# Performance work log

Hardware: AMD Instinct MI355X
Metric: run time of the kernel (lower is better)

Reference implementation:

```python
import jax, jax.numpy as jnp
import numpy as np

T, B, IN, OUT = 32, 16, 64, 64
L, W, S = 4096, 64, 3          # mem_length, mem_width, shifting_size
READ_SIZE = W + 3 + S           # k, beta, g, gamma, s
WRITE_SIZE = W + 3 + S + 2 * W  # addressing params + erase + add


def setup_inputs() -> dict:
    key = jax.random.key(0)
    k1, k2 = jax.random.split(key)
    inputs = jax.random.normal(k1, (T, B, IN), dtype=jnp.float32)
    Wc = jax.random.normal(k2, (IN + OUT + W, OUT + READ_SIZE + WRITE_SIZE), dtype=jnp.float32) * 0.05
    bc = jnp.zeros((OUT + READ_SIZE + WRITE_SIZE,), dtype=jnp.float32)
    return {"inputs": inputs, "Wc": Wc, "bc": bc}


def _get_w(params, w_prev, memory):
    # params: [B, W+3+S]; w_prev: [B, L]; memory: [B, L, W]
    k = params[:, :W]
    beta = jax.nn.softplus(params[:, W])[:, None]
    g = jax.nn.sigmoid(params[:, W + 1])[:, None]
    gamma = jax.nn.softplus(params[:, W + 2])[:, None] + 1.0
    s = jax.nn.softmax(params[:, -S:], axis=-1)
    eps = 1e-14
    norm_k = jnp.sqrt(jnp.sum(k * k, axis=-1, keepdims=True) + eps)    # [B,1]
    norm_mem = jnp.sqrt(jnp.sum(memory * memory, axis=-1) + eps)       # [B,L]
    K = jnp.einsum('blw,bw->bl', memory, k) / (norm_mem * norm_k)      # cosine sim
    w_c = jax.nn.softmax(K * beta, axis=-1)
    w_g = w_c * g + (1.0 - g) * w_prev
    # circular shift: w_tilde[i] = sum_j s[j] * w_g[(i + j - left) mod L]
    left = S // 2
    shifted = jnp.stack([jnp.roll(w_g, left - j, axis=1) for j in range(S)], axis=-1)  # [B,L,S]
    w_tilde = jnp.einsum('bls,bs->bl', shifted, s)
    w = jnp.power(w_tilde, gamma)   # sharpen, gamma >= 1
    return w / jnp.sum(w, axis=1, keepdims=True)


def reference(inputs, Wc, bc):
    Bsz = inputs.shape[1]
    r0 = jnp.zeros((Bsz, W), jnp.float32)
    o0 = jnp.zeros((Bsz, OUT), jnp.float32)
    w0 = jnp.zeros((Bsz, L), jnp.float32).at[:, 0].set(1.0)  # one-hot init weights
    m0 = jnp.zeros((Bsz, L, W), jnp.float32)

    def step(carry, x_t):
        r, out, rw, ww, mem = carry
        co = jnp.concatenate([x_t, out, r], axis=1) @ Wc + bc  # linear controller
        out = co[:, :OUT]
        rp = co[:, OUT:OUT + READ_SIZE]
        wp = co[:, -WRITE_SIZE:]
        # read head (uses pre-write memory)
        rw = _get_w(rp, rw, mem)
        r = jnp.einsum('blw,bl->bw', mem, rw)
        # write head: address with same memory, then erase/add
        ww = _get_w(wp[:, :-2 * W], ww, mem)
        e = jax.nn.sigmoid(wp[:, -2 * W:-W])
        a = wp[:, -W:]
        mem = mem * (1.0 - ww[:, :, None] * e[:, None, :]) + ww[:, :, None] * a[:, None, :]
        return (r, out, rw, ww, mem), out

    _, outs = jax.lax.scan(step, (r0, o0, w0, w0, m0), inputs)
    return outs  # [T, B, OUT]
```

## Files before the change

kernel.cpp:

```cpp
#include <hip/hip_runtime.h>

#define T_STEPS 32
#define BATCH   16
#define NBPB    16
#define NBLK    (BATCH * NBPB)
#define NTHR    1024
#define LSL     256
#define MSTR    65
#define NIN     192
#define CO      332

#define OFF_CTR   0
#define OFF_SSUM  512
#define OFF_RSUM  (OFF_SSUM + BATCH * T_STEPS * 4)
#define OFF_HE    (OFF_RSUM + BATCH * T_STEPS * 64)
#define OFF_HP    (OFF_HE + BATCH * T_STEPS * NBPB * 4)
#define COMM_FLOATS (OFF_HP + BATCH * (T_STEPS + 1) * NBPB * 4)

__device__ __forceinline__ float waveSum(float v) {
#pragma unroll
  for (int off = 32; off > 0; off >>= 1) v += __shfl_xor(v, off, 64);
  return v;
}
__device__ __forceinline__ float sigmoidf(float x) { return 1.f / (1.f + __expf(-x)); }
__device__ __forceinline__ float softplusf(float x) { return x > 15.f ? x : log1pf(__expf(x)); }
__device__ __forceinline__ float aload(const float* p) {
  return __hip_atomic_load(p, __ATOMIC_RELAXED, __HIP_MEMORY_SCOPE_AGENT);
}
__device__ __forceinline__ void astore(float* p, float v) {
  __hip_atomic_store(p, v, __ATOMIC_RELAXED, __HIP_MEMORY_SCOPE_AGENT);
}

__device__ __forceinline__ void gbar(unsigned* c, unsigned expected) {
  __syncthreads();
  if (threadIdx.x == 0) {
    atomicAdd(c, 1u);
    while (__hip_atomic_load(c, __ATOMIC_RELAXED, __HIP_MEMORY_SCOPE_AGENT) < expected)
      __builtin_amdgcn_s_sleep(1);
  }
  __syncthreads();
}

__global__ void __launch_bounds__(NTHR, 1) ntm_kernel(
    const float* __restrict__ inp, const float* __restrict__ Wc,
    const float* __restrict__ bcv, float* __restrict__ dout,
    float* __restrict__ comm)
{
  const int b   = blockIdx.x & 15;
  const int g   = blockIdx.x >> 4;
  const int tid = threadIdx.x;
  const int wv  = tid >> 6;
  const int lane = tid & 63;

  __shared__ float mem[LSL * MSTR];
  __shared__ float wpR[LSL], wpW[LSL];
  __shared__ float wbR[LSL], wbW[LSL];
  __shared__ float erR[LSL], erW[LSL];
  __shared__ float xin[NIN], kr[64], kw[64], psc[12], elds[64], alds[64];
  __shared__ float outb[2][64], scrA[16], scrB[16], red[8], rpart[64];
  __shared__ float edge[8], coef[12];

  unsigned* ctr = (unsigned*)comm + b * 32;

  for (int i = tid; i < LSL * MSTR; i += NTHR) mem[i] = 0.f;
  if (tid < LSL) { wpR[tid] = 0.f; wpW[tid] = 0.f; }
  if (g == 0 && tid == 0) { wpR[0] = 1.f; wpW[0] = 1.f; }
  if (tid < 64) { outb[0][tid] = 0.f; outb[1][tid] = 0.f; }
  {
    float* hp0 = comm + OFF_HP + ((size_t)(b * (T_STEPS + 1) + 0) * NBPB + g) * 4;
    if (tid == 0)       { float v = (g == 0) ? 1.f : 0.f; astore(hp0 + 0, v); astore(hp0 + 2, v); }
    if (tid == LSL - 1) { astore(hp0 + 1, 0.f); astore(hp0 + 3, 0.f); }
  }
  unsigned expct = NBPB;
  gbar(ctr, expct);

  for (int t = 0; t < T_STEPS; ++t) {
    float* sS  = comm + OFF_SSUM + (size_t)(b * T_STEPS + t) * 4;
    float* rS  = comm + OFF_RSUM + (size_t)(b * T_STEPS + t) * 64;
    float* hE  = comm + OFF_HE + ((size_t)(b * T_STEPS + t) * NBPB + g) * 4;
    float* hPn = comm + OFF_HP + ((size_t)(b * (T_STEPS + 1) + t + 1) * NBPB + g) * 4;

    if (tid < 64)       xin[tid] = inp[((size_t)t * BATCH + b) * 64 + tid];
    else if (tid < 128) xin[tid] = outb[(t + 1) & 1][tid - 64];
    else if (tid < 192) {
      if (t == 0) xin[tid] = 0.f;
      else {
        const float* sP = comm + OFF_SSUM + (size_t)(b * T_STEPS + t - 1) * 4;
        const float* rP = comm + OFF_RSUM + (size_t)(b * T_STEPS + t - 1) * 64;
        xin[tid] = aload(rP + (tid - 128)) / aload(sP + 2);
      }
    }
    __syncthreads();

    if (tid < 2 * CO) {
      const int col = tid >> 1, h = tid & 1;
      float acc = h ? 0.f : bcv[col];
      const float* wcp = Wc + col + (size_t)(96 * h) * CO;
#pragma unroll 8
      for (int i = 0; i < 96; ++i) acc = fmaf(xin[96 * h + i], wcp[(size_t)i * CO], acc);
      acc += __shfl_xor(acc, 1, 64);
      if (h == 0) {
        if (col < 64) {
          outb[t & 1][col] = acc;
          if (g == 0) dout[((size_t)t * BATCH + b) * 64 + col] = acc;
        }
        else if (col < 128) kr[col - 64] = acc;
        else if (col < 134) psc[col - 128] = acc;
        else if (col < 198) kw[col - 134] = acc;
        else if (col < 204) psc[6 + (col - 198)] = acc;
        else if (col < 268) elds[col - 204] = sigmoidf(acc);
        else                alds[col - 268] = acc;
      }
    }
    __syncthreads();
    if (wv == 0)      { float v = kr[lane]; float s = waveSum(v * v); if (!lane) red[4] = 1.f / sqrtf(s + 1e-14f); }
    else if (wv == 1) { float v = kw[lane]; float s = waveSum(v * v); if (!lane) red[5] = 1.f / sqrtf(s + 1e-14f); }
    else if (wv == 2 && !lane) { red[6] = softplusf(psc[0]); red[7] = softplusf(psc[6]); }
    __syncthreads();

    {
      const float invnkR = red[4], invnkW = red[5];
      const float betaR = red[6], betaW = red[7];
      const int l = tid >> 2, h = tid & 3;
      const int base = l * MSTR + 16 * h;
      const float* krh = kr + 16 * h;
      const float* kwh = kw + 16 * h;
      float ss = 0.f, dr = 0.f, dw = 0.f;
#pragma unroll 8
      for (int i = 0; i < 16; ++i) {
        float v = mem[base + i];
        ss = fmaf(v, v, ss); dr = fmaf(v, krh[i], dr); dw = fmaf(v, kwh[i], dw);
      }
      ss += __shfl_xor(ss, 1, 64); ss += __shfl_xor(ss, 2, 64);
      dr += __shfl_xor(dr, 1, 64); dr += __shfl_xor(dr, 2, 64);
      dw += __shfl_xor(dw, 1, 64); dw += __shfl_xor(dw, 2, 64);
      float rinv = rsqrtf(ss + 1e-14f);
      float eRv = __expf(betaR * (dr * rinv * invnkR - 1.f));
      float eWv = __expf(betaW * (dw * rinv * invnkW - 1.f));
      if (h == 0) {
        erR[l] = eRv; erW[l] = eWv;
        if (l == 0)       { astore(hE + 0, eRv); astore(hE + 2, eWv); }
        if (l == LSL - 1) { astore(hE + 1, eRv); astore(hE + 3, eWv); }
      }
      float sRl = h ? 0.f : eRv, sWl = h ? 0.f : eWv;
      sRl = waveSum(sRl); sWl = waveSum(sWl);
      if (!lane) { scrA[wv] = sRl; scrB[wv] = sWl; }
      __syncthreads();
      if (tid == 0) {
        float a = 0.f, bb = 0.f;
        for (int j = 0; j < 16; ++j) { a += scrA[j]; bb += scrB[j]; }
        atomicAdd(sS + 0, a); atomicAdd(sS + 1, bb);
      }
    }
    expct += NBPB; gbar(ctr, expct);

    {
      const int gm = (g + NBPB - 1) & (NBPB - 1), gp = (g + 1) & (NBPB - 1);
      if (tid == 0) {
        float invSR = 1.f / aload(sS + 0), invSW = 1.f / aload(sS + 1);
        float gR = sigmoidf(psc[1]); coef[0] = gR * invSR; coef[1] = 1.f - gR;
        coef[2] = softplusf(psc[2]) + 1.f;
        float x0 = psc[3], x1 = psc[4], x2 = psc[5];
        float mx = fmaxf(x0, fmaxf(x1, x2));
        float e0 = __expf(x0 - mx), e1 = __expf(x1 - mx), e2 = __expf(x2 - mx);
        float es = 1.f / (e0 + e1 + e2);
        coef[3] = e0 * es; coef[4] = e1 * es; coef[5] = e2 * es;
        float gW = sigmoidf(psc[7]); coef[6] = gW * invSW; coef[7] = 1.f - gW;
        coef[8] = softplusf(psc[8]) + 1.f;
        float y0 = psc[9], y1 = psc[10], y2 = psc[11];
        float my = fmaxf(y0, fmaxf(y1, y2));
        float f0 = __expf(y0 - my), f1 = __expf(y1 - my), f2 = __expf(y2 - my);
        float fs = 1.f / (f0 + f1 + f2);
        coef[9] = f0 * fs; coef[10] = f1 * fs; coef[11] = f2 * fs;
      }
      if (tid == 1) {
        const float* hEm = comm + OFF_HE + ((size_t)(b * T_STEPS + t) * NBPB + gm) * 4;
        const float* hPm = comm + OFF_HP + ((size_t)(b * (T_STEPS + 1) + t) * NBPB + gm) * 4;
        edge[0] = aload(hEm + 1); edge[1] = aload(hEm + 3);
        edge[2] = aload(hPm + 1); edge[3] = aload(hPm + 3);
      }
      if (tid == 2) {
        const float* hEp = comm + OFF_HE + ((size_t)(b * T_STEPS + t) * NBPB + gp) * 4;
        const float* hPp = comm + OFF_HP + ((size_t)(b * (T_STEPS + 1) + t) * NBPB + gp) * 4;
        edge[4] = aload(hEp + 0); edge[5] = aload(hEp + 2);
        edge[6] = aload(hPp + 0); edge[7] = aload(hPp + 2);
      }
      __syncthreads();

      float pRl = 0.f, pWl = 0.f;
      if (tid < LSL) {
        const float aR = coef[0], bR = coef[1], gaR = coef[2];
        const float sr0 = coef[3], sr1 = coef[4], sr2 = coef[5];
        const float aW = coef[6], bW = coef[7], gaW = coef[8];
        const float sw0 = coef[9], sw1 = coef[10], sw2 = coef[11];

        float erm = tid ? erR[tid - 1] : edge[0];
        float ewm = tid ? erW[tid - 1] : edge[1];
        float prm = tid ? wpR[tid - 1] : edge[2];
        float pwm = tid ? wpW[tid - 1] : edge[3];
        float erp = (tid < LSL - 1) ? erR[tid + 1] : edge[4];
        float ewp = (tid < LSL - 1) ? erW[tid + 1] : edge[5];
        float prp = (tid < LSL - 1) ? wpR[tid + 1] : edge[6];
        float pwp = (tid < LSL - 1) ? wpW[tid + 1] : edge[7];

        float wgm = aR * erm + bR * prm;
        float wg0 = aR * erR[tid] + bR * wpR[tid];
        float wgp = aR * erp + bR * prp;
        float wR = __powf(sr0 * wgm + sr1 * wg0 + sr2 * wgp, gaR);
        float vgm = aW * ewm + bW * pwm;
        float vg0 = aW * erW[tid] + bW * wpW[tid];
        float vgp = aW * ewp + bW * pwp;
        float wW = __powf(sw0 * vgm + sw1 * vg0 + sw2 * vgp, gaW);
        wbR[tid] = wR; wbW[tid] = wW;
        pRl = wR; pWl = wW;
      }
      pRl = waveSum(pRl); pWl = waveSum(pWl);
      if (!lane && wv < 4) { scrA[wv] = pRl; scrB[wv] = pWl; }
      __syncthreads();
      if (tid == 0) {
        float a = 0.f, bb = 0.f;
        for (int j = 0; j < 4; ++j) { a += scrA[j]; bb += scrB[j]; }
        atomicAdd(sS + 2, a); atomicAdd(sS + 3, bb);
      }
      float wbv[4];
#pragma unroll
      for (int k = 0; k < 4; ++k) wbv[k] = wbR[lane + 64 * k];
#pragma unroll
      for (int r2 = 0; r2 < 4; ++r2) {
        const int w = wv * 4 + r2;
        float racc = 0.f;
#pragma unroll
        for (int k = 0; k < 4; ++k)
          racc = fmaf(mem[(lane + 64 * k) * MSTR + w], wbv[k], racc);
        racc = waveSum(racc);
        if (!lane) rpart[w] = racc;
      }
      __syncthreads();
      if (tid < 64) atomicAdd(rS + tid, rpart[tid]);
    }
    expct += NBPB; gbar(ctr, expct);

    {
      if (tid == 0) { red[2] = 1.f / aload(sS + 2); red[3] = 1.f / aload(sS + 3); }
      __syncthreads();
      if (tid < LSL) {
        float nR = wbR[tid] * red[2];
        float nW = wbW[tid] * red[3];
        wpR[tid] = nR; wpW[tid] = nW;
        if (tid == 0)       { astore(hPn + 0, nR); astore(hPn + 2, nW); }
        if (tid == LSL - 1) { astore(hPn + 1, nR); astore(hPn + 3, nW); }
      }
      __syncthreads();
      float wwv[4];
#pragma unroll
      for (int k = 0; k < 4; ++k) wwv[k] = wpW[lane + 64 * k];
#pragma unroll
      for (int r2 = 0; r2 < 4; ++r2) {
        const int w = wv * 4 + r2;
        const float e_w = elds[w], a_w = alds[w];
#pragma unroll
        for (int k = 0; k < 4; ++k) {
          const int idx = (lane + 64 * k) * MSTR + w;
          float v = mem[idx];
          float nv = fmaf(v, -(wwv[k] * e_w), v);
          mem[idx] = fmaf(wwv[k], a_w, nv);
        }
      }
    }
  }
}

extern "C" void kernel_launch(void* const* d_in, const int* in_sizes, int n_in,
                              void* d_out, int out_size, void* d_ws, size_t ws_size,
                              hipStream_t stream) {
  const float* inp = (const float*)d_in[0];
  const float* Wc  = (const float*)d_in[1];
  const float* bcv = (const float*)d_in[2];
  float* dout = (float*)d_out;
  float* comm = (float*)d_ws;

  hipMemsetAsync(comm, 0, (size_t)COMM_FLOATS * sizeof(float), stream);

  void* args[] = { (void*)&inp, (void*)&Wc, (void*)&bcv, (void*)&dout, (void*)&comm };
  hipLaunchCooperativeKernel((void*)ntm_kernel, dim3(NBLK), dim3(NTHR),
                             args, 0, stream);
}
```

Measured before the change: 654.5 us.

## Split each batch row across 32 smaller blocks with double-buffered halo exchange

Each batch element's memory slice is now spread over 32 blocks of 512 threads, 128 rows each, instead of 16 blocks of 1024 threads. The aim is to halve the per-block LDS work and use more CUs. The controller matvec now gives each thread one column with two accumulators instead of pairing threads through a shuffle. The per-timestep halo and edge buffers shrink to a two-slot ring. The launch also switches from a cooperative launch to a plain one. The spin barrier then relies on all 512 blocks being co-resident, and each barrier now has twice as many participants.

```diff
diff --git a/kernel.cpp b/kernel.cpp
--- a/kernel.cpp
+++ b/kernel.cpp
@@ -2,10 +2,10 @@
 
 #define T_STEPS 32
 #define BATCH   16
-#define NBPB    16
+#define NBPB    32
 #define NBLK    (BATCH * NBPB)
-#define NTHR    1024
-#define LSL     256
+#define NTHR    512
+#define LSL     128
 #define MSTR    65
 #define NIN     192
 #define CO      332
@@ -14,8 +14,8 @@
 #define OFF_SSUM  512
 #define OFF_RSUM  (OFF_SSUM + BATCH * T_STEPS * 4)
 #define OFF_HE    (OFF_RSUM + BATCH * T_STEPS * 64)
-#define OFF_HP    (OFF_HE + BATCH * T_STEPS * NBPB * 4)
-#define COMM_FLOATS (OFF_HP + BATCH * (T_STEPS + 1) * NBPB * 4)
+#define OFF_HP    (OFF_HE + BATCH * 2 * NBPB * 4)
+#define COMM_FLOATS (OFF_HP + BATCH * 2 * NBPB * 4)
 
 __device__ __forceinline__ float waveSum(float v) {
 #pragma unroll
@@ -57,7 +57,7 @@
   __shared__ float wbR[LSL], wbW[LSL];
   __shared__ float erR[LSL], erW[LSL];
   __shared__ float xin[NIN], kr[64], kw[64], psc[12], elds[64], alds[64];
-  __shared__ float outb[2][64], scrA[16], scrB[16], red[8], rpart[64];
+  __shared__ float outb[2][64], scrA[8], scrB[8], red[8], rpart[64];
   __shared__ float edge[8], coef[12];
 
   unsigned* ctr = (unsigned*)comm + b * 32;
@@ -67,7 +67,7 @@
   if (g == 0 && tid == 0) { wpR[0] = 1.f; wpW[0] = 1.f; }
   if (tid < 64) { outb[0][tid] = 0.f; outb[1][tid] = 0.f; }
   {
-    float* hp0 = comm + OFF_HP + ((size_t)(b * (T_STEPS + 1) + 0) * NBPB + g) * 4;
+    float* hp0 = comm + OFF_HP + ((size_t)(b * 2 + 0) * NBPB + g) * 4;
     if (tid == 0)       { float v = (g == 0) ? 1.f : 0.f; astore(hp0 + 0, v); astore(hp0 + 2, v); }
     if (tid == LSL - 1) { astore(hp0 + 1, 0.f); astore(hp0 + 3, 0.f); }
   }
@@ -77,8 +77,8 @@
   for (int t = 0; t < T_STEPS; ++t) {
     float* sS  = comm + OFF_SSUM + (size_t)(b * T_STEPS + t) * 4;
     float* rS  = comm + OFF_RSUM + (size_t)(b * T_STEPS + t) * 64;
-    float* hE  = comm + OFF_HE + ((size_t)(b * T_STEPS + t) * NBPB + g) * 4;
-    float* hPn = comm + OFF_HP + ((size_t)(b * (T_STEPS + 1) + t + 1) * NBPB + g) * 4;
+    float* hE  = comm + OFF_HE + ((size_t)(b * 2 + (t & 1)) * NBPB + g) * 4;
+    float* hPn = comm + OFF_HP + ((size_t)(b * 2 + ((t + 1) & 1)) * NBPB + g) * 4;
 
     if (tid < 64)       xin[tid] = inp[((size_t)t * BATCH + b) * 64 + tid];
     else if (tid < 128) xin[tid] = outb[(t + 1) & 1][tid - 64];
@@ -92,25 +92,25 @@
     }
     __syncthreads();
 
-    if (tid < 2 * CO) {
-      const int col = tid >> 1, h = tid & 1;
-      float acc = h ? 0.f : bcv[col];
-      const float* wcp = Wc + col + (size_t)(96 * h) * CO;
+    if (tid < CO) {
+      const float* wcp = Wc + tid;
+      float a0 = bcv[tid], a1 = 0.f;
 #pragma unroll 8
-      for (int i = 0; i < 96; ++i) acc = fmaf(xin[96 * h + i], wcp[(size_t)i * CO], acc);
-      acc += __shfl_xor(acc, 1, 64);
-      if (h == 0) {
-        if (col < 64) {
-          outb[t & 1][col] = acc;
-          if (g == 0) dout[((size_t)t * BATCH + b) * 64 + col] = acc;
-        }
-        else if (col < 128) kr[col - 64] = acc;
-        else if (col < 134) psc[col - 128] = acc;
-        else if (col < 198) kw[col - 134] = acc;
-        else if (col < 204) psc[6 + (col - 198)] = acc;
-        else if (col < 268) elds[col - 204] = sigmoidf(acc);
-        else                alds[col - 268] = acc;
-      }
+      for (int i = 0; i < 96; ++i) {
+        a0 = fmaf(xin[i],      wcp[(size_t)i * CO],        a0);
+        a1 = fmaf(xin[96 + i], wcp[(size_t)(96 + i) * CO], a1);
+      }
+      const float acc = a0 + a1;
+      if (tid < 64) {
+        outb[t & 1][tid] = acc;
+        if (g == 0) dout[((size_t)t * BATCH + b) * 64 + tid] = acc;
+      }
+      else if (tid < 128) kr[tid - 64] = acc;
+      else if (tid < 134) psc[tid - 128] = acc;
+      else if (tid < 198) kw[tid - 134] = acc;
+      else if (tid < 204) psc[6 + (tid - 198)] = acc;
+      else if (tid < 268) elds[tid - 204] = sigmoidf(acc);
+      else                alds[tid - 268] = acc;
     }
     __syncthreads();
     if (wv == 0)      { float v = kr[lane]; float s = waveSum(v * v); if (!lane) red[4] = 1.f / sqrtf(s + 1e-14f); }
@@ -148,7 +148,7 @@
       __syncthreads();
       if (tid == 0) {
         float a = 0.f, bb = 0.f;
-        for (int j = 0; j < 16; ++j) { a += scrA[j]; bb += scrB[j]; }
+        for (int j = 0; j < 8; ++j) { a += scrA[j]; bb += scrB[j]; }
         atomicAdd(sS + 0, a); atomicAdd(sS + 1, bb);
       }
     }
@@ -174,14 +174,14 @@
         coef[9] = f0 * fs; coef[10] = f1 * fs; coef[11] = f2 * fs;
       }
       if (tid == 1) {
-        const float* hEm = comm + OFF_HE + ((size_t)(b * T_STEPS + t) * NBPB + gm) * 4;
-        const float* hPm = comm + OFF_HP + ((size_t)(b * (T_STEPS + 1) + t) * NBPB + gm) * 4;
+        const float* hEm = comm + OFF_HE + ((size_t)(b * 2 + (t & 1)) * NBPB + gm) * 4;
+        const float* hPm = comm + OFF_HP + ((size_t)(b * 2 + (t & 1)) * NBPB + gm) * 4;
         edge[0] = aload(hEm + 1); edge[1] = aload(hEm + 3);
         edge[2] = aload(hPm + 1); edge[3] = aload(hPm + 3);
       }
       if (tid == 2) {
-        const float* hEp = comm + OFF_HE + ((size_t)(b * T_STEPS + t) * NBPB + gp) * 4;
-        const float* hPp = comm + OFF_HP + ((size_t)(b * (T_STEPS + 1) + t) * NBPB + gp) * 4;
+        const float* hEp = comm + OFF_HE + ((size_t)(b * 2 + (t & 1)) * NBPB + gp) * 4;
+        const float* hPp = comm + OFF_HP + ((size_t)(b * 2 + (t & 1)) * NBPB + gp) * 4;
         edge[4] = aload(hEp + 0); edge[5] = aload(hEp + 2);
         edge[6] = aload(hPp + 0); edge[7] = aload(hPp + 2);
       }
@@ -215,22 +215,22 @@
         pRl = wR; pWl = wW;
       }
       pRl = waveSum(pRl); pWl = waveSum(pWl);
-      if (!lane && wv < 4) { scrA[wv] = pRl; scrB[wv] = pWl; }
+      if (!lane && wv < 2) { scrA[wv] = pRl; scrB[wv] = pWl; }
       __syncthreads();
       if (tid == 0) {
         float a = 0.f, bb = 0.f;
-        for (int j = 0; j < 4; ++j) { a += scrA[j]; bb += scrB[j]; }
+        for (int j = 0; j < 2; ++j) { a += scrA[j]; bb += scrB[j]; }
         atomicAdd(sS + 2, a); atomicAdd(sS + 3, bb);
       }
-      float wbv[4];
-#pragma unroll
-      for (int k = 0; k < 4; ++k) wbv[k] = wbR[lane + 64 * k];
-#pragma unroll
-      for (int r2 = 0; r2 < 4; ++r2) {
-        const int w = wv * 4 + r2;
+      float wbv[2];
+#pragma unroll
+      for (int k = 0; k < 2; ++k) wbv[k] = wbR[lane + 64 * k];
+#pragma unroll
+      for (int r2 = 0; r2 < 8; ++r2) {
+        const int w = wv * 8 + r2;
         float racc = 0.f;
 #pragma unroll
-        for (int k = 0; k < 4; ++k)
+        for (int k = 0; k < 2; ++k)
           racc = fmaf(mem[(lane + 64 * k) * MSTR + w], wbv[k], racc);
         racc = waveSum(racc);
         if (!lane) rpart[w] = racc;
@@ -251,15 +251,15 @@
         if (tid == LSL - 1) { astore(hPn + 1, nR); astore(hPn + 3, nW); }
       }
       __syncthreads();
-      float wwv[4];
-#pragma unroll
-      for (int k = 0; k < 4; ++k) wwv[k] = wpW[lane + 64 * k];
-#pragma unroll
-      for (int r2 = 0; r2 < 4; ++r2) {
-        const int w = wv * 4 + r2;
+      float wwv[2];
+#pragma unroll
+      for (int k = 0; k < 2; ++k) wwv[k] = wpW[lane + 64 * k];
+#pragma unroll
+      for (int r2 = 0; r2 < 8; ++r2) {
+        const int w = wv * 8 + r2;
         const float e_w = elds[w], a_w = alds[w];
 #pragma unroll
-        for (int k = 0; k < 4; ++k) {
+        for (int k = 0; k < 2; ++k) {
           const int idx = (lane + 64 * k) * MSTR + w;
           float v = mem[idx];
           float nv = fmaf(v, -(wwv[k] * e_w), v);
@@ -281,7 +281,6 @@
 
   hipMemsetAsync(comm, 0, (size_t)COMM_FLOATS * sizeof(float), stream);
 
-  void* args[] = { (void*)&inp, (void*)&Wc, (void*)&bcv, (void*)&dout, (void*)&comm };
-  hipLaunchCooperativeKernel((void*)ntm_kernel, dim3(NBLK), dim3(NTHR),
-                             args, 0, stream);
-}
+  hipLaunchKernelGGL(ntm_kernel, dim3(NBLK), dim3(NTHR), 0, stream,
+                     inp, Wc, bcv, dout, comm);
+}
```

New measurement: 715.2 us. 1.09x slower.
